# Kernel tuning notes

Hardware: AMD Instinct MI355X
Metric: run time of the kernel (lower is better)

## Reference

```python
import jax, jax.numpy as jnp
import numpy as np

N = 100000   # nodes
E = 3200000  # edges
G = 256      # graphs in batch
C_IN, H, OUT = 5, 64, 2
EPS = 1e-5


def setup_inputs() -> dict:
    key = jax.random.key(0)
    ks = jax.random.split(key, 16)
    d = {
        "x": jax.random.normal(ks[0], (N, C_IN), jnp.float32),
        "edge_index": jax.random.randint(ks[1], (2, E), 0, N, jnp.int64),
        "batch": jnp.sort(jax.random.randint(ks[2], (N,), 0, G, jnp.int64)),
        "W1": jax.random.normal(ks[3], (C_IN, H), jnp.float32),
        "b1": jax.random.normal(ks[4], (H,), jnp.float32),
        "g1": jax.random.uniform(ks[5], (H,), jnp.float32),
        "be1": jax.random.normal(ks[6], (H,), jnp.float32),
        "rm1": jnp.zeros((H,), jnp.float32),
        "rv1": jnp.ones((H,), jnp.float32),
        "W2": jax.random.normal(ks[7], (H, H), jnp.float32),
        "b2": jax.random.normal(ks[8], (H,), jnp.float32),
        "g2": jax.random.uniform(ks[9], (H,), jnp.float32),
        "be2": jax.random.normal(ks[10], (H,), jnp.float32),
        "rm2": jnp.zeros((H,), jnp.float32),
        "rv2": jnp.ones((H,), jnp.float32),
        "W3": jax.random.normal(ks[11], (H, H), jnp.float32),
        "b3": jax.random.normal(ks[12], (H,), jnp.float32),
        "g3": jax.random.uniform(ks[13], (H,), jnp.float32),
        "be3": jax.random.normal(ks[14], (H,), jnp.float32),
        "rm3": jnp.zeros((H,), jnp.float32),
        "rv3": jnp.ones((H,), jnp.float32),
        "Wf1": jax.random.normal(ks[15], (H, 32), jnp.float32),
        "bf1": jax.random.normal(jax.random.fold_in(key, 1), (32,), jnp.float32),
        "Wf2": jax.random.normal(jax.random.fold_in(key, 2), (32, OUT), jnp.float32),
        "bf2": jax.random.normal(jax.random.fold_in(key, 3), (OUT,), jnp.float32),
    }
    return d


def reference(x, edge_index, batch, W1, b1, g1, be1, rm1, rv1,
              W2, b2, g2, be2, rm2, rv2, W3, b3, g3, be3, rm3, rv3,
              Wf1, bf1, Wf2, bf2):
    src, dst = edge_index[0], edge_index[1]
    # GCN symmetric normalization with self-loops: deg includes the self edge
    deg = jax.ops.segment_sum(jnp.ones((E,), x.dtype), dst, num_segments=N) + 1.0
    dinv = jax.lax.rsqrt(deg)            # [N]
    enorm = dinv[src] * dinv[dst]        # per-edge norm  [E]
    snorm = dinv * dinv                  # self-loop norm [N]

    def gcn(h, W, b):
        h = h @ W                                                  # [N,H]
        agg = jax.ops.segment_sum(h[src] * enorm[:, None], dst, num_segments=N)
        return agg + h * snorm[:, None] + b

    def bn(h, g, be, rm, rv):  # eval-mode BatchNorm1d
        return (h - rm) * jax.lax.rsqrt(rv + EPS) * g + be

    h = jax.nn.relu(bn(gcn(x, W1, b1), g1, be1, rm1, rv1))
    h = jax.nn.relu(bn(gcn(h, W2, b2), g2, be2, rm2, rv2))
    h = jax.nn.relu(bn(gcn(h, W3, b3), g3, be3, rm3, rv3))

    counts = jax.ops.segment_sum(jnp.ones((N,), h.dtype), batch, num_segments=G)
    pooled = jax.ops.segment_sum(h, batch, num_segments=G) / jnp.maximum(counts, 1.0)[:, None]

    h = jax.nn.relu(pooled @ Wf1 + bf1)  # dropout is identity in eval
    return jax.nn.sigmoid(h @ Wf2 + bf2)
```

## Files before the change

### kernel.cpp

```cpp
#include <hip/hip_runtime.h>
#include <hip/hip_bf16.h>

#define HF 64
#define EPS 1e-5f

#define BSH 9
#define BKN (1 << BSH)
#define NBUCK_MAX 256
#define PB_T 256
#define PB_EPT 32
#define PB_TILE (PB_T * PB_EPT)

#define LGRID 2048

typedef __hip_bfloat16 bf16;

__device__ __forceinline__ unsigned char f32_to_fp8(float v) {
    int p = __builtin_amdgcn_cvt_pk_fp8_f32(v, v, 0, false);
    return (unsigned char)(p & 0xff);
}

__device__ __forceinline__ float rdlane(float v, int k) {
    return __int_as_float(__builtin_amdgcn_readlane(__float_as_int(v), k));
}

__device__ __forceinline__ unsigned bf16_rne_hi(float x) {
    unsigned u = __float_as_uint(x);
    return (u + 0x7fffu + ((u >> 16) & 1u)) & 0xffff0000u;
}

__global__ __launch_bounds__(PB_T) void k_bhist(const int* __restrict__ dst,
                                                int* __restrict__ bcnt, int E, int B) {
    __shared__ int bh[NBUCK_MAX];
    int t = threadIdx.x;
    for (int b = t; b < B; b += PB_T) bh[b] = 0;
    __syncthreads();
    int tile0 = blockIdx.x * PB_TILE;
#pragma unroll
    for (int k = 0; k < PB_EPT; ++k) {
        int e = tile0 + k * PB_T + t;
        if (e < E) atomicAdd(&bh[dst[e] >> BSH], 1);
    }
    __syncthreads();
    for (int b = t; b < B; b += PB_T) {
        int c = bh[b];
        if (c) atomicAdd(&bcnt[b], c);
    }
}

__global__ void k_bscan(const int* __restrict__ bcnt, int* __restrict__ bbase2,
                        int* __restrict__ bcur, int* __restrict__ base, int B, int N, int E) {
    if (threadIdx.x == 0 && blockIdx.x == 0) {
        int acc = 0;
        for (int i = 0; i < B; ++i) { bbase2[i] = acc; bcur[i] = acc; acc += bcnt[i]; }
        bbase2[B] = acc;
        base[N] = E;
    }
}

__global__ __launch_bounds__(PB_T) void k_passB(
    const int* __restrict__ src, const int* __restrict__ dst,
    int* __restrict__ bcur, int* __restrict__ stage, int E, int B) {
    __shared__ int scnt[NBUCK_MAX];
    __shared__ int sgoff[NBUCK_MAX];
    int t = threadIdx.x;
    int tile0 = blockIdx.x * PB_TILE;

    for (int b = t; b < B; b += PB_T) scnt[b] = 0;
    __syncthreads();

    int rec[PB_EPT];
    int bkt[PB_EPT];
#pragma unroll
    for (int k = 0; k < PB_EPT; ++k) {
        int e = tile0 + k * PB_T + t;
        bkt[k] = -1;
        if (e < E) {
            int d = dst[e];
            int s = src[e];
            int b = d >> BSH;
            bkt[k] = b;
            rec[k] = s | ((d & (BKN - 1)) << 17);
            atomicAdd(&scnt[b], 1);
        }
    }
    __syncthreads();

    for (int b = t; b < B; b += PB_T) {
        int c = scnt[b];
        sgoff[b] = c ? atomicAdd(&bcur[b], c) : 0;
        scnt[b] = 0;
    }
    __syncthreads();

#pragma unroll
    for (int k = 0; k < PB_EPT; ++k) {
        if (bkt[k] >= 0) {
            int loc = atomicAdd(&scnt[bkt[k]], 1);
            stage[sgoff[bkt[k]] + loc] = rec[k];
        }
    }
}

__global__ __launch_bounds__(512) void k_passC(const int* __restrict__ stage,
                                               const int* __restrict__ bb2,
                                               int* __restrict__ base,
                                               float* __restrict__ dinv,
                                               int* __restrict__ csr, int N) {
    __shared__ int lcnt[BKN];
    __shared__ int lscan[BKN];
    __shared__ int lcur[BKN];
    int beta = blockIdx.x;
    int n0 = beta * BKN;
    int n1 = n0 + BKN; if (n1 > N) n1 = N;
    int nn = n1 - n0;
    int t = threadIdx.x;
    lcnt[t] = 0;
    __syncthreads();
    int rbeg = bb2[beta], rend = bb2[beta + 1];
    for (int i = rbeg + t; i < rend; i += 512)
        atomicAdd(&lcnt[stage[i] >> 17], 1);
    __syncthreads();
    int v = lcnt[t];
    lscan[t] = v;
    __syncthreads();
    for (int off = 1; off < 512; off <<= 1) {
        int val = lscan[t];
        int add = (t >= off) ? lscan[t - off] : 0;
        __syncthreads();
        lscan[t] = val + add;
        __syncthreads();
    }
    int b = rbeg + lscan[t] - v;
    if (t < nn) {
        base[n0 + t] = b;
        dinv[n0 + t] = rsqrtf((float)v + 1.0f);
    }
    lcur[t] = b;
    __syncthreads();
    for (int i = rbeg + t; i < rend; i += 512) {
        int r = stage[i];
        int pos = atomicAdd(&lcur[r >> 17], 1);
        csr[pos] = r & 0x1ffff;
    }
}

__global__ void k_prescale(const float* __restrict__ x, const float* __restrict__ dinv,
                           float* __restrict__ xs, int N5) {
    int i = blockIdx.x * blockDim.x + threadIdx.x;
    if (i < N5) xs[i] = x[i] * dinv[i / 5];
}

__global__ __launch_bounds__(256) void k_layer1(
    const float* __restrict__ xs, unsigned char* __restrict__ hout,
    const int* __restrict__ csr, const int* __restrict__ basep,
    const float* __restrict__ dinv,
    const float* __restrict__ W1, const float* __restrict__ b,
    const float* __restrict__ g, const float* __restrict__ be,
    const float* __restrict__ rm, const float* __restrict__ rv, int N) {
    __shared__ float sW[5 * HF];
    __shared__ float sB[HF];
    __shared__ float sScale[HF];
    if (threadIdx.x < HF) {
        int f = threadIdx.x;
        float scale = g[f] * rsqrtf(rv[f] + EPS);
        sScale[f] = scale;
        sB[f] = (b[f] - rm[f]) * scale + be[f];
    }
    __syncthreads();
    for (int i = threadIdx.x; i < 5 * HF; i += blockDim.x)
        sW[i] = W1[i] * sScale[i & (HF - 1)];
    __syncthreads();

    int lane = threadIdx.x & 63;
    int wave = threadIdx.x >> 6;
    int c  = lane & 7;
    int g8 = lane >> 3;
    int stride = gridDim.x * 4;

    for (int node = blockIdx.x * 4 + wave; node < N; node += stride) {
        int j   = __builtin_amdgcn_readfirstlane(basep[node]);
        int end = __builtin_amdgcn_readfirstlane(basep[node + 1]);

        float a0 = 0.f, a1 = 0.f, a2 = 0.f, a3 = 0.f;
        if (g8 == 0 && c < 5) a0 = xs[node * 5 + c];

        for (; j + 32 <= end; j += 32) {
            int s0 = csr[j + g8];
            int s1 = csr[j + 8 + g8];
            int s2 = csr[j + 16 + g8];
            int s3 = csr[j + 24 + g8];
            float v0 = xs[s0 * 5 + c];
            float v1 = xs[s1 * 5 + c];
            float v2 = xs[s2 * 5 + c];
            float v3 = xs[s3 * 5 + c];
            a0 += v0; a1 += v1; a2 += v2; a3 += v3;
        }
        for (; j + 8 <= end; j += 8) {
            int s = csr[j + g8];
            a0 += xs[s * 5 + c];
        }
        if (j < end) {
            if (j + g8 < end) {
                int s = csr[j + g8];
                a0 += xs[s * 5 + c];
            }
        }

        float acc = (a0 + a1) + (a2 + a3);
        acc += __shfl_xor(acc, 8, 64);
        acc += __shfl_xor(acc, 16, 64);
        acc += __shfl_xor(acc, 32, 64);

        float di = dinv[node];
        acc *= di;

        float out = sB[lane];
#pragma unroll
        for (int k = 0; k < 5; ++k) out += __shfl(acc, k, 64) * sW[k * HF + lane];
        out = fmaxf(out, 0.f);
        hout[(size_t)node * HF + lane] = f32_to_fp8(out * di);
    }
}

template <int SCALE_OUT>
__global__ __launch_bounds__(256, 4) void k_layer(
    const unsigned char* __restrict__ hs8, void* __restrict__ hout_v,
    const int* __restrict__ csr, const int* __restrict__ basep,
    const float* __restrict__ dinv,
    const float* __restrict__ W, const float* __restrict__ b,
    const float* __restrict__ g, const float* __restrict__ be,
    const float* __restrict__ rm, const float* __restrict__ rv, int N) {
    __shared__ uint4 swp4[64][8];

    int lane = threadIdx.x & 63;
    int wave = threadIdx.x >> 6;
    int stride = gridDim.x * 4;
    const unsigned char* col = hs8 + lane;

    if (threadIdx.x < 64) {
        int l = threadIdx.x;
        float sc = g[l] * rsqrtf(rv[l] + EPS);
#pragma unroll
        for (int c = 0; c < 8; ++c) {
            unsigned p[4];
#pragma unroll
            for (int q = 0; q < 4; ++q) {
                int k2 = c * 4 + q;
                unsigned lo = bf16_rne_hi(W[(2 * k2 + 0) * HF + l] * sc);
                unsigned hi = bf16_rne_hi(W[(2 * k2 + 1) * HF + l] * sc);
                p[q] = (lo >> 16) | hi;
            }
            swp4[l][c ^ (l & 7)] = make_uint4(p[0], p[1], p[2], p[3]);
        }
    }
    __syncthreads();

    float scale = g[lane] * rsqrtf(rv[lane] + EPS);
    float bias  = (b[lane] - rm[lane]) * scale + be[lane];

    auto mlp_store = [&](float acc, int nodeS, float diS) {
        float o0 = bias, o1 = 0.f, o2 = 0.f, o3 = 0.f;
#pragma unroll
        for (int c = 0; c < 8; ++c) {
            uint4 pv = swp4[lane][c ^ (lane & 7)];
            int k0 = c * 8;
            o0 += rdlane(acc, k0 + 0) * __uint_as_float(pv.x << 16);
            o1 += rdlane(acc, k0 + 1) * __uint_as_float(pv.x & 0xffff0000u);
            o2 += rdlane(acc, k0 + 2) * __uint_as_float(pv.y << 16);
            o3 += rdlane(acc, k0 + 3) * __uint_as_float(pv.y & 0xffff0000u);
            o0 += rdlane(acc, k0 + 4) * __uint_as_float(pv.z << 16);
            o1 += rdlane(acc, k0 + 5) * __uint_as_float(pv.z & 0xffff0000u);
            o2 += rdlane(acc, k0 + 6) * __uint_as_float(pv.w << 16);
            o3 += rdlane(acc, k0 + 7) * __uint_as_float(pv.w & 0xffff0000u);
        }
        float out = fmaxf((o0 + o1) + (o2 + o3), 0.f);
        if (SCALE_OUT) {
            ((unsigned char*)hout_v)[(size_t)nodeS * HF + lane] = f32_to_fp8(out * diS);
        } else {
            ((float*)hout_v)[(size_t)nodeS * HF + lane] = out;
        }
    };

    float accP = 0.f, diP = 0.f;
    int nodeP = -1;

    for (int node = blockIdx.x * 4 + wave; node < N; node += stride) {
        int j   = __builtin_amdgcn_readfirstlane(basep[node]);
        int end = __builtin_amdgcn_readfirstlane(basep[node + 1]);

        float a0 = __builtin_amdgcn_cvt_f32_fp8((unsigned)col[(size_t)node * HF], 0);
        float a1 = 0.f, a2 = 0.f, a3 = 0.f;

        unsigned u0 = 0, u1 = 0, u2 = 0, u3 = 0, u4 = 0, u5 = 0, u6 = 0, u7 = 0;
        bool w0 = (j + 8 <= end);
        if (w0) {
            int s0 = csr[j+0], s1 = csr[j+1], s2 = csr[j+2], s3 = csr[j+3];
            int s4 = csr[j+4], s5 = csr[j+5], s6 = csr[j+6], s7 = csr[j+7];
            u0 = col[(size_t)s0 * HF]; u1 = col[(size_t)s1 * HF];
            u2 = col[(size_t)s2 * HF]; u3 = col[(size_t)s3 * HF];
            u4 = col[(size_t)s4 * HF]; u5 = col[(size_t)s5 * HF];
            u6 = col[(size_t)s6 * HF]; u7 = col[(size_t)s7 * HF];
        }

        if (nodeP >= 0) mlp_store(accP, nodeP, diP);

        if (w0) {
            j += 8;
            while (j + 8 <= end) {
                int t0 = csr[j+0], t1 = csr[j+1], t2 = csr[j+2], t3 = csr[j+3];
                int t4 = csr[j+4], t5 = csr[j+5], t6 = csr[j+6], t7 = csr[j+7];
                unsigned v0 = col[(size_t)t0 * HF];
                unsigned v1 = col[(size_t)t1 * HF];
                unsigned v2 = col[(size_t)t2 * HF];
                unsigned v3 = col[(size_t)t3 * HF];
                unsigned v4 = col[(size_t)t4 * HF];
                unsigned v5 = col[(size_t)t5 * HF];
                unsigned v6 = col[(size_t)t6 * HF];
                unsigned v7 = col[(size_t)t7 * HF];
                a0 += __builtin_amdgcn_cvt_f32_fp8(u0, 0);
                a1 += __builtin_amdgcn_cvt_f32_fp8(u1, 0);
                a2 += __builtin_amdgcn_cvt_f32_fp8(u2, 0);
                a3 += __builtin_amdgcn_cvt_f32_fp8(u3, 0);
                a0 += __builtin_amdgcn_cvt_f32_fp8(u4, 0);
                a1 += __builtin_amdgcn_cvt_f32_fp8(u5, 0);
                a2 += __builtin_amdgcn_cvt_f32_fp8(u6, 0);
                a3 += __builtin_amdgcn_cvt_f32_fp8(u7, 0);
                u0 = v0; u1 = v1; u2 = v2; u3 = v3;
                u4 = v4; u5 = v5; u6 = v6; u7 = v7;
                j += 8;
            }
            a0 += __builtin_amdgcn_cvt_f32_fp8(u0, 0);
            a1 += __builtin_amdgcn_cvt_f32_fp8(u1, 0);
            a2 += __builtin_amdgcn_cvt_f32_fp8(u2, 0);
            a3 += __builtin_amdgcn_cvt_f32_fp8(u3, 0);
            a0 += __builtin_amdgcn_cvt_f32_fp8(u4, 0);
            a1 += __builtin_amdgcn_cvt_f32_fp8(u5, 0);
            a2 += __builtin_amdgcn_cvt_f32_fp8(u6, 0);
            a3 += __builtin_amdgcn_cvt_f32_fp8(u7, 0);
        }
        for (; j < end; ++j) {
            int s = csr[j];
            a0 += __builtin_amdgcn_cvt_f32_fp8((unsigned)col[(size_t)s * HF], 0);
        }

        float di = dinv[node];
        accP = ((a0 + a1) + (a2 + a3)) * di;
        diP = di;
        nodeP = node;
    }
    if (nodeP >= 0) mlp_store(accP, nodeP, diP);
}

__global__ void k_pool_fc(const float* __restrict__ h, const int* __restrict__ batch,
                          const float* __restrict__ Wf1, const float* __restrict__ bf1,
                          const float* __restrict__ Wf2, const float* __restrict__ bf2,
                          float* __restrict__ out, int N) {
    int g = blockIdx.x;
    int t = threadIdx.x;
    int f = t & 63, q = t >> 6;

    int lo = 0, hi = N;
    while (lo < hi) { int mid = (lo + hi) >> 1; if (batch[mid] < g) lo = mid + 1; else hi = mid; }
    int start = lo;
    hi = N;
    while (lo < hi) { int mid = (lo + hi) >> 1; if (batch[mid] < g + 1) lo = mid + 1; else hi = mid; }
    int end = lo;

    float sum = 0.f;
    for (int n = start + q; n < end; n += 4) sum += h[n * HF + f];

    __shared__ float red[4][HF];
    __shared__ float sp[HF];
    __shared__ float sh[32];
    red[q][f] = sum;
    __syncthreads();
    if (q == 0) {
        float s = red[0][f] + red[1][f] + red[2][f] + red[3][f];
        float cntf = (float)(end - start);
        sp[f] = s / fmaxf(cntf, 1.0f);
    }
    __syncthreads();
    if (t < 32) {
        float a = bf1[t];
#pragma unroll
        for (int k = 0; k < HF; ++k) a += sp[k] * Wf1[k * 32 + t];
        sh[t] = fmaxf(a, 0.f);
    }
    __syncthreads();
    if (t < 2) {
        float a = bf2[t];
#pragma unroll
        for (int k = 0; k < 32; ++k) a += sh[k] * Wf2[k * 2 + t];
        out[g * 2 + t] = 1.f / (1.f + expf(-a));
    }
}

extern "C" void kernel_launch(void* const* d_in, const int* in_sizes, int n_in,
                              void* d_out, int out_size, void* d_ws, size_t ws_size,
                              hipStream_t stream) {
    const float* x     = (const float*)d_in[0];
    const int*   ei    = (const int*)d_in[1];
    const int*   batch = (const int*)d_in[2];
    const float* W1 = (const float*)d_in[3];
    const float* b1 = (const float*)d_in[4];
    const float* g1 = (const float*)d_in[5];
    const float* be1 = (const float*)d_in[6];
    const float* rm1 = (const float*)d_in[7];
    const float* rv1 = (const float*)d_in[8];
    const float* W2 = (const float*)d_in[9];
    const float* b2 = (const float*)d_in[10];
    const float* g2 = (const float*)d_in[11];
    const float* be2 = (const float*)d_in[12];
    const float* rm2 = (const float*)d_in[13];
    const float* rv2 = (const float*)d_in[14];
    const float* W3 = (const float*)d_in[15];
    const float* b3 = (const float*)d_in[16];
    const float* g3 = (const float*)d_in[17];
    const float* be3 = (const float*)d_in[18];
    const float* rm3 = (const float*)d_in[19];
    const float* rv3 = (const float*)d_in[20];
    const float* Wf1 = (const float*)d_in[21];
    const float* bf1 = (const float*)d_in[22];
    const float* Wf2 = (const float*)d_in[23];
    const float* bf2 = (const float*)d_in[24];
    float* out = (float*)d_out;

    const int N = in_sizes[2];
    const int E = in_sizes[1] / 2;
    const int G = out_size / 2;
    const int B = (N + BKN - 1) / BKN;

    char* ws = (char*)d_ws;
    size_t off = 0;
    auto alloc = [&](size_t bytes) {
        char* p = ws + off;
        off += (bytes + 255) & ~(size_t)255;
        return p;
    };
    float*         H3       = (float*)alloc((size_t)N * HF * sizeof(float));
    unsigned char* HS1      = (unsigned char*)alloc((size_t)N * HF);
    unsigned char* HS2      = (unsigned char*)alloc((size_t)N * HF);
    float*         xs       = (float*)alloc((size_t)N * 5 * sizeof(float) + 64);
    float*         dinv     = (float*)alloc((size_t)N * sizeof(float));
    int*           base     = (int*)  alloc(((size_t)N + 1) * sizeof(int));
    int*           bcnt     = (int*)  alloc((size_t)NBUCK_MAX * sizeof(int));
    int*           bbase2   = (int*)  alloc(((size_t)NBUCK_MAX + 1) * sizeof(int));
    int*           bcur     = (int*)  alloc((size_t)NBUCK_MAX * sizeof(int));
    int*           csr      = (int*)  alloc((size_t)E * sizeof(int));
    int*           stage    = (int*)H3;

    const int* src = ei;
    const int* dst = ei + E;

    const int BT = 256;
    int gP  = (N * 5 + BT - 1) / BT;
    int gPB = (E + PB_TILE - 1) / PB_TILE;

    hipMemsetAsync(bcnt, 0, (size_t)B * sizeof(int), stream);
    k_bhist<<<gPB, PB_T, 0, stream>>>(dst, bcnt, E, B);
    k_bscan<<<1, 64, 0, stream>>>(bcnt, bbase2, bcur, base, B, N, E);
    k_passB<<<gPB, PB_T, 0, stream>>>(src, dst, bcur, stage, E, B);
    k_passC<<<B, 512, 0, stream>>>(stage, bbase2, base, dinv, csr, N);
    k_prescale<<<gP, BT, 0, stream>>>(x, dinv, xs, N * 5);

    k_layer1<<<LGRID, BT, 0, stream>>>(xs, HS1, csr, base, dinv,
                                       W1, b1, g1, be1, rm1, rv1, N);
    k_layer<1><<<LGRID, BT, 0, stream>>>(HS1, HS2, csr, base, dinv,
                                         W2, b2, g2, be2, rm2, rv2, N);
    k_layer<0><<<LGRID, BT, 0, stream>>>(HS2, H3, csr, base, dinv,
                                         W3, b3, g3, be3, rm3, rv3, N);

    k_pool_fc<<<G, BT, 0, stream>>>(H3, batch, Wf1, bf1, Wf2, bf2, out, N);
}
```

Baseline: 427.5 us.

## Drop separate histogram pass via per-block bucket table; software-pipeline layer1 gather

The CSR build no longer runs a global histogram pass, a serial scan and atomic bucket cursors. Each block now sorts its tile locally into stage and records per-bucket offsets and counts in a table, a small kernel scans the totals, and passC reads each bucket's segments straight from the table. This saves one full read of dst and the global atomics, at the cost of strided segment reads in passC and a larger table. Layer1 also delays each node's MLP/store so it overlaps with the next node's gather loads, and the layer's LDS weight swizzle is swapped for a padded row stride.

After: 504.9 us. +18.1%, slower.

```diff
diff --git a/kernel.cpp b/kernel.cpp
--- a/kernel.cpp
+++ b/kernel.cpp
@@ -29,44 +29,16 @@
     return (u + 0x7fffu + ((u >> 16) & 1u)) & 0xffff0000u;
 }
 
-__global__ __launch_bounds__(PB_T) void k_bhist(const int* __restrict__ dst,
-                                                int* __restrict__ bcnt, int E, int B) {
-    __shared__ int bh[NBUCK_MAX];
+__global__ __launch_bounds__(PB_T) void k_passB2(
+    const int* __restrict__ src, const int* __restrict__ dst,
+    int* __restrict__ stage, unsigned* __restrict__ rtab, int E, int B) {
+    __shared__ int scnt[NBUCK_MAX];
+    __shared__ int sscan[PB_T];
     int t = threadIdx.x;
-    for (int b = t; b < B; b += PB_T) bh[b] = 0;
-    __syncthreads();
-    int tile0 = blockIdx.x * PB_TILE;
-#pragma unroll
-    for (int k = 0; k < PB_EPT; ++k) {
-        int e = tile0 + k * PB_T + t;
-        if (e < E) atomicAdd(&bh[dst[e] >> BSH], 1);
-    }
-    __syncthreads();
-    for (int b = t; b < B; b += PB_T) {
-        int c = bh[b];
-        if (c) atomicAdd(&bcnt[b], c);
-    }
-}
-
-__global__ void k_bscan(const int* __restrict__ bcnt, int* __restrict__ bbase2,
-                        int* __restrict__ bcur, int* __restrict__ base, int B, int N, int E) {
-    if (threadIdx.x == 0 && blockIdx.x == 0) {
-        int acc = 0;
-        for (int i = 0; i < B; ++i) { bbase2[i] = acc; bcur[i] = acc; acc += bcnt[i]; }
-        bbase2[B] = acc;
-        base[N] = E;
-    }
-}
-
-__global__ __launch_bounds__(PB_T) void k_passB(
-    const int* __restrict__ src, const int* __restrict__ dst,
-    int* __restrict__ bcur, int* __restrict__ stage, int E, int B) {
-    __shared__ int scnt[NBUCK_MAX];
-    __shared__ int sgoff[NBUCK_MAX];
-    int t = threadIdx.x;
-    int tile0 = blockIdx.x * PB_TILE;
-
-    for (int b = t; b < B; b += PB_T) scnt[b] = 0;
+    int blk = blockIdx.x;
+    int tile0 = blk * PB_TILE;
+
+    for (int b = t; b < NBUCK_MAX; b += PB_T) scnt[b] = 0;
     __syncthreads();
 
     int rec[PB_EPT];
@@ -86,10 +58,20 @@
     }
     __syncthreads();
 
-    for (int b = t; b < B; b += PB_T) {
-        int c = scnt[b];
-        sgoff[b] = c ? atomicAdd(&bcur[b], c) : 0;
-        scnt[b] = 0;
+    int v = (t < B) ? scnt[t] : 0;
+    sscan[t] = v;
+    __syncthreads();
+    for (int off = 1; off < PB_T; off <<= 1) {
+        int val = sscan[t];
+        int add = (t >= off) ? sscan[t - off] : 0;
+        __syncthreads();
+        sscan[t] = val + add;
+        __syncthreads();
+    }
+    int excl = sscan[t] - v;
+    if (t < B) {
+        rtab[(size_t)blk * B + t] = ((unsigned)excl << 14) | (unsigned)v;
+        scnt[t] = excl;
     }
     __syncthreads();
 
@@ -97,16 +79,39 @@
     for (int k = 0; k < PB_EPT; ++k) {
         if (bkt[k] >= 0) {
             int loc = atomicAdd(&scnt[bkt[k]], 1);
-            stage[sgoff[bkt[k]] + loc] = rec[k];
-        }
-    }
-}
-
-__global__ __launch_bounds__(512) void k_passC(const int* __restrict__ stage,
-                                               const int* __restrict__ bb2,
-                                               int* __restrict__ base,
-                                               float* __restrict__ dinv,
-                                               int* __restrict__ csr, int N) {
+            stage[tile0 + loc] = rec[k];
+        }
+    }
+}
+
+__global__ void k_bscan2(const unsigned* __restrict__ rtab, int* __restrict__ bbase2,
+                         int* __restrict__ base, int B, int nblk, int N, int E) {
+    __shared__ int tot[NBUCK_MAX];
+    int t = threadIdx.x;
+    int s = 0;
+    if (t < B)
+        for (int blk = 0; blk < nblk; ++blk)
+            s += (int)(rtab[(size_t)blk * B + t] & 0x3FFFu);
+    tot[t] = s;
+    __syncthreads();
+    for (int off = 1; off < 256; off <<= 1) {
+        int val = tot[t];
+        int add = (t >= off) ? tot[t - off] : 0;
+        __syncthreads();
+        tot[t] = val + add;
+        __syncthreads();
+    }
+    if (t < B) bbase2[t] = tot[t] - s;
+    if (t == 0) { bbase2[B] = E; base[N] = E; }
+}
+
+__global__ __launch_bounds__(512) void k_passC2(const int* __restrict__ stage,
+                                                const unsigned* __restrict__ rtab,
+                                                const int* __restrict__ bb2,
+                                                int* __restrict__ base,
+                                                float* __restrict__ dinv,
+                                                int* __restrict__ csr,
+                                                int N, int B, int nblk) {
     __shared__ int lcnt[BKN];
     __shared__ int lscan[BKN];
     __shared__ int lcur[BKN];
@@ -115,11 +120,21 @@
     int n1 = n0 + BKN; if (n1 > N) n1 = N;
     int nn = n1 - n0;
     int t = threadIdx.x;
+    int rg = t >> 4;
+    int le = t & 15;
     lcnt[t] = 0;
     __syncthreads();
-    int rbeg = bb2[beta], rend = bb2[beta + 1];
-    for (int i = rbeg + t; i < rend; i += 512)
-        atomicAdd(&lcnt[stage[i] >> 17], 1);
+
+    for (int blk0 = 0; blk0 < nblk; blk0 += 32) {
+        int blk = blk0 + rg;
+        if (blk < nblk) {
+            unsigned rt = rtab[(size_t)blk * B + beta];
+            int cnt = (int)(rt & 0x3FFFu);
+            int off = blk * PB_TILE + (int)(rt >> 14);
+            for (int i = le; i < cnt; i += 16)
+                atomicAdd(&lcnt[stage[off + i] >> 17], 1);
+        }
+    }
     __syncthreads();
     int v = lcnt[t];
     lscan[t] = v;
@@ -131,17 +146,26 @@
         lscan[t] = val + add;
         __syncthreads();
     }
-    int b = rbeg + lscan[t] - v;
+    int b = bb2[beta] + lscan[t] - v;
     if (t < nn) {
         base[n0 + t] = b;
         dinv[n0 + t] = rsqrtf((float)v + 1.0f);
     }
     lcur[t] = b;
     __syncthreads();
-    for (int i = rbeg + t; i < rend; i += 512) {
-        int r = stage[i];
-        int pos = atomicAdd(&lcur[r >> 17], 1);
-        csr[pos] = r & 0x1ffff;
+
+    for (int blk0 = 0; blk0 < nblk; blk0 += 32) {
+        int blk = blk0 + rg;
+        if (blk < nblk) {
+            unsigned rt = rtab[(size_t)blk * B + beta];
+            int cnt = (int)(rt & 0x3FFFu);
+            int off = blk * PB_TILE + (int)(rt >> 14);
+            for (int i = le; i < cnt; i += 16) {
+                int r = stage[off + i];
+                int pos = atomicAdd(&lcur[r >> 17], 1);
+                csr[pos] = r & 0x1ffff;
+            }
+        }
     }
 }
 
@@ -178,6 +202,17 @@
     int g8 = lane >> 3;
     int stride = gridDim.x * 4;
 
+    auto mlp_store = [&](float accS, int nodeS, float diS) {
+        float out = sB[lane];
+#pragma unroll
+        for (int k = 0; k < 5; ++k) out += __shfl(accS, k, 64) * sW[k * HF + lane];
+        out = fmaxf(out, 0.f);
+        hout[(size_t)nodeS * HF + lane] = f32_to_fp8(out * diS);
+    };
+
+    float accP = 0.f, diP = 0.f;
+    int nodeP = -1;
+
     for (int node = blockIdx.x * 4 + wave; node < N; node += stride) {
         int j   = __builtin_amdgcn_readfirstlane(basep[node]);
         int end = __builtin_amdgcn_readfirstlane(basep[node + 1]);
@@ -185,26 +220,43 @@
         float a0 = 0.f, a1 = 0.f, a2 = 0.f, a3 = 0.f;
         if (g8 == 0 && c < 5) a0 = xs[node * 5 + c];
 
-        for (; j + 32 <= end; j += 32) {
+        float u0 = 0.f, u1 = 0.f, u2 = 0.f, u3 = 0.f;
+        bool w0 = (j + 32 <= end);
+        if (w0) {
             int s0 = csr[j + g8];
             int s1 = csr[j + 8 + g8];
             int s2 = csr[j + 16 + g8];
             int s3 = csr[j + 24 + g8];
-            float v0 = xs[s0 * 5 + c];
-            float v1 = xs[s1 * 5 + c];
-            float v2 = xs[s2 * 5 + c];
-            float v3 = xs[s3 * 5 + c];
-            a0 += v0; a1 += v1; a2 += v2; a3 += v3;
+            u0 = xs[s0 * 5 + c]; u1 = xs[s1 * 5 + c];
+            u2 = xs[s2 * 5 + c]; u3 = xs[s3 * 5 + c];
+        }
+
+        if (nodeP >= 0) mlp_store(accP, nodeP, diP);
+
+        if (w0) {
+            j += 32;
+            while (j + 32 <= end) {
+                int s0 = csr[j + g8];
+                int s1 = csr[j + 8 + g8];
+                int s2 = csr[j + 16 + g8];
+                int s3 = csr[j + 24 + g8];
+                float v0 = xs[s0 * 5 + c];
+                float v1 = xs[s1 * 5 + c];
+                float v2 = xs[s2 * 5 + c];
+                float v3 = xs[s3 * 5 + c];
+                a0 += u0; a1 += u1; a2 += u2; a3 += u3;
+                u0 = v0; u1 = v1; u2 = v2; u3 = v3;
+                j += 32;
+            }
+            a0 += u0; a1 += u1; a2 += u2; a3 += u3;
         }
         for (; j + 8 <= end; j += 8) {
             int s = csr[j + g8];
             a0 += xs[s * 5 + c];
         }
-        if (j < end) {
-            if (j + g8 < end) {
-                int s = csr[j + g8];
-                a0 += xs[s * 5 + c];
-            }
+        if (j < end && j + g8 < end) {
+            int s = csr[j + g8];
+            a0 += xs[s * 5 + c];
         }
 
         float acc = (a0 + a1) + (a2 + a3);
@@ -213,14 +265,11 @@
         acc += __shfl_xor(acc, 32, 64);
 
         float di = dinv[node];
-        acc *= di;
-
-        float out = sB[lane];
-#pragma unroll
-        for (int k = 0; k < 5; ++k) out += __shfl(acc, k, 64) * sW[k * HF + lane];
-        out = fmaxf(out, 0.f);
-        hout[(size_t)node * HF + lane] = f32_to_fp8(out * di);
-    }
+        accP = acc * di;
+        diP = di;
+        nodeP = node;
+    }
+    if (nodeP >= 0) mlp_store(accP, nodeP, diP);
 }
 
 template <int SCALE_OUT>
@@ -231,7 +280,7 @@
     const float* __restrict__ W, const float* __restrict__ b,
     const float* __restrict__ g, const float* __restrict__ be,
     const float* __restrict__ rm, const float* __restrict__ rv, int N) {
-    __shared__ uint4 swp4[64][8];
+    __shared__ uint4 swp4[64][9];
 
     int lane = threadIdx.x & 63;
     int wave = threadIdx.x >> 6;
@@ -251,7 +300,7 @@
                 unsigned hi = bf16_rne_hi(W[(2 * k2 + 1) * HF + l] * sc);
                 p[q] = (lo >> 16) | hi;
             }
-            swp4[l][c ^ (l & 7)] = make_uint4(p[0], p[1], p[2], p[3]);
+            swp4[l][c] = make_uint4(p[0], p[1], p[2], p[3]);
         }
     }
     __syncthreads();
@@ -263,7 +312,7 @@
         float o0 = bias, o1 = 0.f, o2 = 0.f, o3 = 0.f;
 #pragma unroll
         for (int c = 0; c < 8; ++c) {
-            uint4 pv = swp4[lane][c ^ (lane & 7)];
+            uint4 pv = swp4[lane][c];
             int k0 = c * 8;
             o0 += rdlane(acc, k0 + 0) * __uint_as_float(pv.x << 16);
             o1 += rdlane(acc, k0 + 1) * __uint_as_float(pv.x & 0xffff0000u);
@@ -438,15 +487,16 @@
         off += (bytes + 255) & ~(size_t)255;
         return p;
     };
+    const int nblk = (E + PB_TILE - 1) / PB_TILE;
+
     float*         H3       = (float*)alloc((size_t)N * HF * sizeof(float));
     unsigned char* HS1      = (unsigned char*)alloc((size_t)N * HF);
     unsigned char* HS2      = (unsigned char*)alloc((size_t)N * HF);
     float*         xs       = (float*)alloc((size_t)N * 5 * sizeof(float) + 64);
     float*         dinv     = (float*)alloc((size_t)N * sizeof(float));
     int*           base     = (int*)  alloc(((size_t)N + 1) * sizeof(int));
-    int*           bcnt     = (int*)  alloc((size_t)NBUCK_MAX * sizeof(int));
     int*           bbase2   = (int*)  alloc(((size_t)NBUCK_MAX + 1) * sizeof(int));
-    int*           bcur     = (int*)  alloc((size_t)NBUCK_MAX * sizeof(int));
+    unsigned*      rtab     = (unsigned*)alloc((size_t)nblk * B * sizeof(unsigned));
     int*           csr      = (int*)  alloc((size_t)E * sizeof(int));
     int*           stage    = (int*)H3;
 
@@ -455,13 +505,10 @@
 
     const int BT = 256;
     int gP  = (N * 5 + BT - 1) / BT;
-    int gPB = (E + PB_TILE - 1) / PB_TILE;
-
-    hipMemsetAsync(bcnt, 0, (size_t)B * sizeof(int), stream);
-    k_bhist<<<gPB, PB_T, 0, stream>>>(dst, bcnt, E, B);
-    k_bscan<<<1, 64, 0, stream>>>(bcnt, bbase2, bcur, base, B, N, E);
-    k_passB<<<gPB, PB_T, 0, stream>>>(src, dst, bcur, stage, E, B);
-    k_passC<<<B, 512, 0, stream>>>(stage, bbase2, base, dinv, csr, N);
+
+    k_passB2<<<nblk, PB_T, 0, stream>>>(src, dst, stage, rtab, E, B);
+    k_bscan2<<<1, 256, 0, stream>>>(rtab, bbase2, base, B, nblk, N, E);
+    k_passC2<<<B, 512, 0, stream>>>(stage, rtab, bbase2, base, dinv, csr, N, B, nblk);
     k_prescale<<<gP, BT, 0, stream>>>(x, dinv, xs, N * 5);
 
     k_layer1<<<LGRID, BT, 0, stream>>>(xs, HS1, csr, base, dinv,
```
